# Performance work log

Measured on AMD Instinct MI355X. Metric: run time of the kernel, lower is better.

The kernel has to match this reference:

```python
import jax, jax.numpy as jnp
import numpy as np

WIRE_DIM = 32
NUM_WIRES = 64
BATCH = 8192


def setup_inputs() -> dict:
    key = jax.random.key(0)
    k1, k2, k3, k4 = jax.random.split(key, 4)
    outputs = jax.random.normal(k1, (BATCH, NUM_WIRES * WIRE_DIM), dtype=jnp.float32)
    tests = jax.random.randint(k2, (BATCH, 2), 0, NUM_WIRES, dtype=jnp.int64)
    W1 = jax.random.normal(k3, (2 * WIRE_DIM, 10), dtype=jnp.float32) * 0.1
    b1 = jnp.zeros((10,), dtype=jnp.float32)
    W2 = jax.random.normal(k4, (10, 1), dtype=jnp.float32) * 0.1
    b2 = jnp.zeros((1,), dtype=jnp.float32)
    return {"outputs": outputs, "tests": tests, "W1": W1, "b1": b1, "W2": W2, "b2": b2}


def reference(outputs, tests, W1, b1, W2, b2):
    B = outputs.shape[0]
    W = outputs.shape[1] // WIRE_DIM          # num_wires
    wires = outputs.reshape(B, W, WIRE_DIM)   # [B, W, D]
    person = tests[:, 0]
    location = tests[:, 1]
    # gather_nd equivalent: person wire vector per batch element
    person_vec = wires[jnp.arange(B), person]                 # [B, D]
    # per-wire concat [person_vec, wire_vec] -> shared tiny MLP, vectorized over wires
    x = jnp.concatenate(
        [jnp.broadcast_to(person_vec[:, None, :], (B, W, WIRE_DIM)), wires], axis=-1
    )                                                          # [B, W, 2D]
    h = jax.nn.relu(jnp.einsum("bwd,dh->bwh", x, W1) + b1)     # [B, W, 10]
    logits = (jnp.einsum("bwh,ho->bwo", h, W2) + b2)[..., 0]   # [B, W]
    # sparse softmax cross entropy with location labels
    loss = -jnp.take_along_axis(jax.nn.log_softmax(logits, axis=-1),
                                location[:, None], axis=-1)[:, 0]  # [B]
    return loss
```

## Files before the change

kernel.cpp:

```cpp
#include <hip/hip_runtime.h>

#define WIRE_DIM  32
#define NUM_WIRES 64
#define BATCH     8192
#define HID       10
#define STRIDE    36

__device__ __forceinline__ float rl(float x, int slane) {
    return __uint_as_float(__builtin_amdgcn_readlane(__float_as_uint(x), slane));
}

__global__ __launch_bounds__(256) void isnet_kernel(
    const float* __restrict__ outputs,
    const int*   __restrict__ tests,
    const float* __restrict__ W1,
    const float* __restrict__ b1,
    const float* __restrict__ W2,
    const float* __restrict__ b2,
    float*       __restrict__ out)
{
    __shared__ __align__(16) float stage[4][NUM_WIRES * STRIDE];

    const int tid  = threadIdx.x;
    const int lane = tid & 63;
    const int wave = tid >> 6;
    float* buf = stage[wave];

    const int b = blockIdx.x * 4 + wave;

    const int sp = __builtin_amdgcn_readfirstlane(tests[2 * b]);
    const int sl = __builtin_amdgcn_readfirstlane(tests[2 * b + 1]);

    const float* grow = outputs + (size_t)b * (NUM_WIRES * WIRE_DIM);
    {
        const int r = lane >> 3;
        const int c = lane & 7;
        #pragma unroll
        for (int t = 0; t < 8; ++t) {
            float4 v = *(const float4*)(grow + t * 256 + lane * 4);
            *(float4*)&buf[(t * 8 + r) * STRIDE + c * 4] = v;
        }
    }

    float acc[HID];
    #pragma unroll
    for (int h = 0; h < HID; ++h) acc[h] = b1[h];

    #pragma unroll 1
    for (int j = 0; j < 8; ++j) {
        float4 x = *(const float4*)&buf[lane * STRIDE + j * 4];
        float4 p = *(const float4*)&buf[sp   * STRIDE + j * 4];
        const float* wp = W1 + (4 * j) * HID;
        const float* ww = W1 + (32 + 4 * j) * HID;
        #pragma unroll
        for (int h = 0; h < HID; ++h) {
            acc[h] += p.x * wp[0 * HID + h] + p.y * wp[1 * HID + h]
                    + p.z * wp[2 * HID + h] + p.w * wp[3 * HID + h]
                    + x.x * ww[0 * HID + h] + x.y * ww[1 * HID + h]
                    + x.z * ww[2 * HID + h] + x.w * ww[3 * HID + h];
        }
    }

    float v = b2[0];
    #pragma unroll
    for (int h = 0; h < HID; ++h) v += fmaxf(acc[h], 0.f) * W2[h];

    float m = v;
    #pragma unroll
    for (int off = 32; off > 0; off >>= 1) m = fmaxf(m, __shfl_xor(m, off));
    float s = __expf(v - m);
    #pragma unroll
    for (int off = 32; off > 0; off >>= 1) s += __shfl_xor(s, off);
    float lv = rl(v, sl);
    if (lane == 0) out[b] = m + __logf(s) - lv;
}

extern "C" void kernel_launch(void* const* d_in, const int* in_sizes, int n_in,
                              void* d_out, int out_size, void* d_ws, size_t ws_size,
                              hipStream_t stream) {
    const float* outputs = (const float*)d_in[0];
    const int*   tests   = (const int*)d_in[1];
    const float* W1      = (const float*)d_in[2];
    const float* b1      = (const float*)d_in[3];
    const float* W2      = (const float*)d_in[4];
    const float* b2      = (const float*)d_in[5];
    float* out = (float*)d_out;

    isnet_kernel<<<BATCH / 4, 256, 0, stream>>>(
        outputs, tests, W1, b1, W2, b2, out);
}
```

Measured before the change: 103.3 us.

## Process two batch rows per wave with register prefetch of second row

Each wave now handles two batch elements, half the grid size. The second row is loaded into registers before the first row's MLP runs, so its global load latency overlaps with the compute. This costs extra registers for the float4 buffer and leaves fewer waves to hide latency through occupancy.

```diff
diff --git a/kernel.cpp b/kernel.cpp
--- a/kernel.cpp
+++ b/kernel.cpp
@@ -5,6 +5,7 @@
 #define BATCH     8192
 #define HID       10
 #define STRIDE    36
+#define NWAVES    4096
 
 __device__ __forceinline__ float rl(float x, int slane) {
     return __uint_as_float(__builtin_amdgcn_readlane(__float_as_uint(x), slane));
@@ -14,9 +15,9 @@
     const float* __restrict__ outputs,
     const int*   __restrict__ tests,
     const float* __restrict__ W1,
-    const float* __restrict__ b1,
+    const float* __restrict__ bias1,
     const float* __restrict__ W2,
-    const float* __restrict__ b2,
+    const float* __restrict__ bias2,
     float*       __restrict__ out)
 {
     __shared__ __align__(16) float stage[4][NUM_WIRES * STRIDE];
@@ -26,53 +27,68 @@
     const int wave = tid >> 6;
     float* buf = stage[wave];
 
-    const int b = blockIdx.x * 4 + wave;
+    const int w0 = blockIdx.x * 4 + wave;
+    const int r  = lane >> 3;
+    const int cc = lane & 7;
 
-    const int sp = __builtin_amdgcn_readfirstlane(tests[2 * b]);
-    const int sl = __builtin_amdgcn_readfirstlane(tests[2 * b + 1]);
+    auto run = [&](int bb) {
+        const int sp = __builtin_amdgcn_readfirstlane(tests[2 * bb]);
+        const int sl = __builtin_amdgcn_readfirstlane(tests[2 * bb + 1]);
 
-    const float* grow = outputs + (size_t)b * (NUM_WIRES * WIRE_DIM);
-    {
-        const int r = lane >> 3;
-        const int c = lane & 7;
+        float acc[HID];
         #pragma unroll
-        for (int t = 0; t < 8; ++t) {
-            float4 v = *(const float4*)(grow + t * 256 + lane * 4);
-            *(float4*)&buf[(t * 8 + r) * STRIDE + c * 4] = v;
+        for (int h = 0; h < HID; ++h) acc[h] = bias1[h];
+
+        #pragma unroll 1
+        for (int j = 0; j < 8; ++j) {
+            float4 x = *(const float4*)&buf[lane * STRIDE + j * 4];
+            float4 p = *(const float4*)&buf[sp   * STRIDE + j * 4];
+            const float* wp = W1 + (4 * j) * HID;
+            const float* ww = W1 + (32 + 4 * j) * HID;
+            #pragma unroll
+            for (int h = 0; h < HID; ++h) {
+                acc[h] += p.x * wp[0 * HID + h] + p.y * wp[1 * HID + h]
+                        + p.z * wp[2 * HID + h] + p.w * wp[3 * HID + h]
+                        + x.x * ww[0 * HID + h] + x.y * ww[1 * HID + h]
+                        + x.z * ww[2 * HID + h] + x.w * ww[3 * HID + h];
+            }
         }
-    }
 
-    float acc[HID];
+        float v = bias2[0];
+        #pragma unroll
+        for (int h = 0; h < HID; ++h) v += fmaxf(acc[h], 0.f) * W2[h];
+
+        float m = v;
+        #pragma unroll
+        for (int off = 32; off > 0; off >>= 1) m = fmaxf(m, __shfl_xor(m, off));
+        float s = __expf(v - m);
+        #pragma unroll
+        for (int off = 32; off > 0; off >>= 1) s += __shfl_xor(s, off);
+        float lv = rl(v, sl);
+        if (lane == 0) out[bb] = m + __logf(s) - lv;
+    };
+
+    float4 c[8];
+
+    const float* g1 = outputs + (size_t)w0 * (NUM_WIRES * WIRE_DIM) + lane * 4;
     #pragma unroll
-    for (int h = 0; h < HID; ++h) acc[h] = b1[h];
+    for (int t = 0; t < 8; ++t) c[t] = *(const float4*)(g1 + t * 256);
+    #pragma unroll
+    for (int t = 0; t < 8; ++t)
+        *(float4*)&buf[(t * 8 + r) * STRIDE + cc * 4] = c[t];
 
-    #pragma unroll 1
-    for (int j = 0; j < 8; ++j) {
-        float4 x = *(const float4*)&buf[lane * STRIDE + j * 4];
-        float4 p = *(const float4*)&buf[sp   * STRIDE + j * 4];
-        const float* wp = W1 + (4 * j) * HID;
-        const float* ww = W1 + (32 + 4 * j) * HID;
-        #pragma unroll
-        for (int h = 0; h < HID; ++h) {
-            acc[h] += p.x * wp[0 * HID + h] + p.y * wp[1 * HID + h]
-                    + p.z * wp[2 * HID + h] + p.w * wp[3 * HID + h]
-                    + x.x * ww[0 * HID + h] + x.y * ww[1 * HID + h]
-                    + x.z * ww[2 * HID + h] + x.w * ww[3 * HID + h];
-        }
-    }
+    const float* g2 = outputs + (size_t)(w0 + NWAVES) * (NUM_WIRES * WIRE_DIM)
+                    + lane * 4;
+    #pragma unroll
+    for (int t = 0; t < 8; ++t) c[t] = *(const float4*)(g2 + t * 256);
 
-    float v = b2[0];
+    run(w0);
+
     #pragma unroll
-    for (int h = 0; h < HID; ++h) v += fmaxf(acc[h], 0.f) * W2[h];
+    for (int t = 0; t < 8; ++t)
+        *(float4*)&buf[(t * 8 + r) * STRIDE + cc * 4] = c[t];
 
-    float m = v;
-    #pragma unroll
-    for (int off = 32; off > 0; off >>= 1) m = fmaxf(m, __shfl_xor(m, off));
-    float s = __expf(v - m);
-    #pragma unroll
-    for (int off = 32; off > 0; off >>= 1) s += __shfl_xor(s, off);
-    float lv = rl(v, sl);
-    if (lane == 0) out[b] = m + __logf(s) - lv;
+    run(w0 + NWAVES);
 }
 
 extern "C" void kernel_launch(void* const* d_in, const int* in_sizes, int n_in,
@@ -86,6 +102,6 @@
     const float* b2      = (const float*)d_in[5];
     float* out = (float*)d_out;
 
-    isnet_kernel<<<BATCH / 4, 256, 0, stream>>>(
+    isnet_kernel<<<NWAVES / 4, 256, 0, stream>>>(
         outputs, tests, W1, b1, W2, b2, out);
 }
```

Measured after the change: 102.7 us. No clear change (-0.5%).
